# Performance work log

Hardware: AMD Instinct MI355X
Metric: run time of the kernel (lower is better)

## Reference

```python
import jax, jax.numpy as jnp
import numpy as np


def setup_inputs() -> dict:
    key = jax.random.key(0)
    k1, k2 = jax.random.split(key)
    x = jax.random.normal(k1, (16, 1024, 256), dtype=jnp.float32)
    codebooks = jax.random.normal(k2, (8, 1024, 256), dtype=jnp.float32)
    return {"x": x, "codebooks": codebooks}


def _mse(a, b):
    return jnp.mean((a - b) ** 2)


def reference(x, codebooks):
    b, s, d = x.shape
    num_codebooks = codebooks.shape[0]
    xf = x.reshape(-1, d)  # [N, d], N = b*s
    res = xf
    quant = jnp.zeros_like(xf)
    loss_cd = jnp.float32(0.0)
    loss_enc = jnp.float32(0.0)
    encs = []
    for i in range(num_codebooks):  # small fixed loop over sequential RVQ stages
        cb = codebooks[i]  # [cd_size, d]
        # squared euclidean distance; argmin is invariant to the sqrt in cdist(p=2)
        d2 = (jnp.sum(res * res, axis=-1, keepdims=True)
              - 2.0 * (res @ cb.T)
              + jnp.sum(cb * cb, axis=-1))  # [N, cd_size]
        enc = jnp.argmin(d2, axis=-1)  # [N]
        nearest = cb[enc]  # [N, d]
        loss_cd = loss_cd + _mse(jax.lax.stop_gradient(res), nearest)
        loss_enc = loss_enc + _mse(res, jax.lax.stop_gradient(nearest))
        res = res - nearest
        quant = quant + nearest
        encs.append(enc)
    discrete_enc = jnp.stack(encs, axis=-1).astype(jnp.float32).reshape(b, s, num_codebooks)
    # straight-through: quantised = residual + sg(quant - residual)
    quantised = res + jax.lax.stop_gradient(quant - res)
    return loss_cd, loss_enc, discrete_enc, quantised.reshape(b, s, d)
```

## Files before the change

kernel.cpp:

```cpp
#include <hip/hip_runtime.h>


#define D 256
#define NCB 1024
#define NROW 16384
#define STAGES 8
#define NELEM 4194304
#define ENC_OFF 2
#define QUANT_OFF 131074

#define SBR 64
#define SBC 128
#define KD 32
#define APITCH 260
#define BPITCH 36

__device__ __forceinline__ double wave_sum(double t) {
#pragma unroll
    for (int off = 1; off < 64; off <<= 1) t += __shfl_xor(t, off);
    return t;
}

__global__ __launch_bounds__(256)
void cn_kernel(const float* __restrict__ cb_all, double* __restrict__ cn64,
               float* __restrict__ cn32) {
    int c = blockIdx.x * 256 + threadIdx.x;
    const float* row = cb_all + (size_t)c * D;
    double s = 0.0;
    for (int k = 0; k < D; ++k) { double a = (double)row[k]; s = fma(a, a, s); }
    cn64[c] = s;
    cn32[c] = (float)s;
}

__global__ __launch_bounds__(256, 1)
void screen_kernel(const float* __restrict__ resv, const float* __restrict__ cbs,
                   const float* __restrict__ cn32s, int2* __restrict__ ti_buf) {
    __shared__ float a_t[SBR * APITCH];
    __shared__ float b_t[2][SBC * BPITCH];

    const int tid = threadIdx.x;
    const int tc  = tid & 15;
    const int tr  = tid >> 4;
    const int k4  = tid & 7;
    const int cb0 = tid >> 3;
    const long rowbase = (long)blockIdx.x * SBR;

#pragma unroll
    for (int i = 0; i < 16; ++i) {
        int e4 = tid + 256 * i;
        int r = e4 >> 6, kk = e4 & 63;
        *(float4*)&a_t[r * APITCH + kk * 4] =
            *(const float4*)(resv + (rowbase + r) * D + kk * 4);
    }

    float4 P0, P1, P2, P3;
#define BFETCH(T) do { int cc_ = (T) >> 3, dc_ = (T) & 7;                    \
        const float* s_ = cbs + (size_t)(cc_ * SBC) * D + dc_ * KD + k4 * 4; \
        P0 = *(const float4*)(s_ + (size_t)(cb0     ) * D);                  \
        P1 = *(const float4*)(s_ + (size_t)(cb0 + 32) * D);                  \
        P2 = *(const float4*)(s_ + (size_t)(cb0 + 64) * D);                  \
        P3 = *(const float4*)(s_ + (size_t)(cb0 + 96) * D); } while (0)
#define BCOMMIT(BUF) do { float* d_ = &b_t[BUF][cb0 * BPITCH + k4 * 4];      \
        *(float4*)(d_               ) = P0;                                  \
        *(float4*)(d_ + 32 * BPITCH ) = P1;                                  \
        *(float4*)(d_ + 64 * BPITCH ) = P2;                                  \
        *(float4*)(d_ + 96 * BPITCH ) = P3; } while (0)

    BFETCH(0);
    BCOMMIT(0);

    float ts1[4], ts2[4]; int ti1[4], ti2[4];
#pragma unroll
    for (int i = 0; i < 4; ++i) { ts1[i] = 3.4e38f; ts2[i] = 3.4e38f; ti1[i] = 0; ti2[i] = 0; }

    for (int cc = 0; cc < 8; ++cc) {
        float acc[4][8];
#pragma unroll
        for (int i = 0; i < 4; ++i)
#pragma unroll
            for (int j = 0; j < 8; ++j) acc[i][j] = 0.f;

        for (int dc = 0; dc < 8; ++dc) {
            const int t = cc * 8 + dc;
            __syncthreads();
            if (t < 63) BFETCH(t + 1);

            const float* bb   = b_t[t & 1];
            const float* arow = &a_t[(tr * 4) * APITCH + dc * KD];
#pragma unroll
            for (int kq = 0; kq < 8; ++kq) {
                float4 A[4], B[8];
#pragma unroll
                for (int i = 0; i < 4; ++i)
                    A[i] = *(const float4*)&arow[i * APITCH + kq * 4];
#pragma unroll
                for (int j = 0; j < 8; ++j)
                    B[j] = *(const float4*)&bb[(j * 16 + tc) * BPITCH + kq * 4];
#pragma unroll
                for (int i = 0; i < 4; ++i)
#pragma unroll
                    for (int j = 0; j < 8; ++j) {
                        acc[i][j] = fmaf(A[i].x, B[j].x, acc[i][j]);
                        acc[i][j] = fmaf(A[i].y, B[j].y, acc[i][j]);
                        acc[i][j] = fmaf(A[i].z, B[j].z, acc[i][j]);
                        acc[i][j] = fmaf(A[i].w, B[j].w, acc[i][j]);
                    }
            }
            if (t < 63) BCOMMIT((t + 1) & 1);
        }

#pragma unroll
        for (int j = 0; j < 8; ++j) {
            int c = cc * SBC + j * 16 + tc;
            float cnv = cn32s[c];
#pragma unroll
            for (int i = 0; i < 4; ++i) {
                float s = cnv - 2.0f * acc[i][j];
                if (s < ts1[i])      { ts2[i] = ts1[i]; ti2[i] = ti1[i]; ts1[i] = s; ti1[i] = c; }
                else if (s < ts2[i]) { ts2[i] = s; ti2[i] = c; }
            }
        }
    }

#pragma unroll
    for (int off = 1; off < 16; off <<= 1) {
#pragma unroll
        for (int i = 0; i < 4; ++i) {
            float os1 = __shfl_xor(ts1[i], off); int oi1 = __shfl_xor(ti1[i], off);
            float os2 = __shfl_xor(ts2[i], off); int oi2 = __shfl_xor(ti2[i], off);
            float a1 = ts1[i], a2 = ts2[i]; int b1 = ti1[i], b2 = ti2[i];
            if (os1 < a1 || (os1 == a1 && oi1 < b1)) { a2 = a1; b2 = b1; a1 = os1; b1 = oi1; }
            else if (os1 < a2 || (os1 == a2 && oi1 < b2)) { a2 = os1; b2 = oi1; }
            if (os2 < a1 || (os2 == a1 && oi2 < b1)) { a2 = a1; b2 = b1; a1 = os2; b1 = oi2; }
            else if (os2 < a2 || (os2 == a2 && oi2 < b2)) { a2 = os2; b2 = oi2; }
            ts1[i] = a1; ti1[i] = b1; ts2[i] = a2; ti2[i] = b2;
        }
    }
    if (tc == 0) {
#pragma unroll
        for (int i = 0; i < 4; ++i)
            ti_buf[rowbase + tr * 4 + i] = make_int2(ti1[i], ti2[i]);
    }
}

__global__ __launch_bounds__(256)
void rescue_kernel(const float* __restrict__ x, const float* __restrict__ cb_all,
                   const double* __restrict__ cn64s, const int2* __restrict__ ti_buf,
                   float* __restrict__ out, double* __restrict__ loss_acc, int stage) {
    const int lane = threadIdx.x & 63;
    const long row = (long)blockIdx.x * 4 + (threadIdx.x >> 6);
    float* encf  = out + ENC_OFF;
    float* res32 = out + QUANT_OFF;

    double v[4];
    {
        float4 xv = *(const float4*)(x + row * D + lane * 4);
        v[0] = xv.x; v[1] = xv.y; v[2] = xv.z; v[3] = xv.w;
    }
    for (int j = 0; j < stage; ++j) {
        int e = (int)encf[row * STAGES + j];
        float4 c4 = *(const float4*)(cb_all + ((size_t)j * NCB + e) * D + lane * 4);
        v[0] -= (double)c4.x; v[1] -= (double)c4.y; v[2] -= (double)c4.z; v[3] -= (double)c4.w;
    }
    double rn = wave_sum(((v[0]*v[0] + v[1]*v[1]) + (v[2]*v[2] + v[3]*v[3])));

    const int2 cand = ti_buf[row];
    const float4 cb0 = *(const float4*)(cb_all + ((size_t)stage * NCB + cand.x) * D + lane * 4);
    const float4 cb1 = *(const float4*)(cb_all + ((size_t)stage * NCB + cand.y) * D + lane * 4);
    double p0 = fma(v[0], (double)cb0.x, fma(v[1], (double)cb0.y,
                fma(v[2], (double)cb0.z, v[3] * (double)cb0.w)));
    double p1 = fma(v[0], (double)cb1.x, fma(v[1], (double)cb1.y,
                fma(v[2], (double)cb1.z, v[3] * (double)cb1.w)));
    double dot0 = wave_sum(p0);
    double dot1 = wave_sum(p1);
    double dA = (rn - 2.0 * dot0) + cn64s[cand.x];
    double dB = (rn - 2.0 * dot1) + cn64s[cand.y];

    double b1, b2; int j1, j2;
    if (dB < dA || (dB == dA && cand.y < cand.x)) { b1 = dB; j1 = cand.y; b2 = dA; j2 = cand.x; }
    else                                          { b1 = dA; j1 = cand.x; b2 = dB; j2 = cand.y; }
    double delta = ldexp(1.0, ilogb(b1) - 23);
    int chosen = j1; double cd2 = b1;
    if ((b2 - b1) < delta && j2 < j1) { chosen = j2; cd2 = b2; }

    float4 cc4 = (chosen == cand.x) ? cb0 : cb1;
    float4 o;
    o.x = (float)(v[0] - (double)cc4.x);
    o.y = (float)(v[1] - (double)cc4.y);
    o.z = (float)(v[2] - (double)cc4.z);
    o.w = (float)(v[3] - (double)cc4.w);
    *(float4*)(res32 + row * D + lane * 4) = o;

    if (lane == 0) {
        encf[row * STAGES + stage] = (float)chosen;
        atomicAdd(loss_acc, cd2);
    }
}

__global__ __launch_bounds__(256)
void final_kernel(const float* __restrict__ x, const double* __restrict__ acc,
                  float* __restrict__ out) {
    long i0 = (long)blockIdx.x * 256 + threadIdx.x;
    if (i0 == 0) {
        float l = (float)(acc[0] / (double)NELEM);
        out[0] = l;
        out[1] = l;
    }
    float* q = out + QUANT_OFF;
    long stride = (long)gridDim.x * 256;
    for (long e = i0; e < NELEM / 4; e += stride) {
        float4 xv = ((const float4*)x)[e];
        float4 rv = ((const float4*)q)[e];
        float4 o;
        o.x = xv.x - rv.x; o.y = xv.y - rv.y; o.z = xv.z - rv.z; o.w = xv.w - rv.w;
        ((float4*)q)[e] = o;
    }
}

extern "C" void kernel_launch(void* const* d_in, const int* in_sizes, int n_in,
                              void* d_out, int out_size, void* d_ws, size_t ws_size,
                              hipStream_t stream) {
    const float* x  = (const float*)d_in[0];
    const float* cb = (const float*)d_in[1];
    float* out = (float*)d_out;

    double* cn64     = (double*)d_ws;
    float*  cn32     = (float*)(cn64 + 8192);
    int2*   ti_buf   = (int2*)(cn32 + 8192);
    double* loss_acc = (double*)(ti_buf + NROW);

    hipMemsetAsync(loss_acc, 0, sizeof(double), stream);
    cn_kernel<<<32, 256, 0, stream>>>(cb, cn64, cn32);

    for (int s = 0; s < STAGES; ++s) {
        const float* resv = (s == 0) ? x : (out + QUANT_OFF);
        screen_kernel<<<NROW / SBR, 256, 0, stream>>>(
            resv, cb + (size_t)s * NCB * D, cn32 + s * NCB, ti_buf);
        rescue_kernel<<<NROW / 4, 256, 0, stream>>>(
            x, cb, cn64 + s * NCB, ti_buf, out, loss_acc, s);
    }

    final_kernel<<<2048, 256, 0, stream>>>(x, loss_acc, out);
}
```

Before: 3.583 ms.

## Shrink screen tiles for occupancy and replace per-row loss atomics with array reduce

The screen kernel's row tile is halved to 32 rows, with threads remapped to 8x32 and a 4x4 register tile instead of 4x8. This doubles the grid to 512 blocks and allows two blocks per CU, the aim being better occupancy on many CUs at the cost of less register reuse per B load. The rescue kernel now loads its earlier encodings up front into an unrolled array, and writes per-row losses to a buffer instead of issuing a double atomicAdd per row. A separate reduction kernel then sums that buffer, which removes atomic contention but adds a launch and extra workspace.

Result: faster. 3.506 ms (-2.1%).

```diff
diff --git a/kernel.cpp b/kernel.cpp
--- a/kernel.cpp
+++ b/kernel.cpp
@@ -9,7 +9,7 @@
 #define ENC_OFF 2
 #define QUANT_OFF 131074
 
-#define SBR 64
+#define SBR 32
 #define SBC 128
 #define KD 32
 #define APITCH 260
@@ -32,21 +32,21 @@
     cn32[c] = (float)s;
 }
 
-__global__ __launch_bounds__(256, 1)
+__global__ __launch_bounds__(256, 2)
 void screen_kernel(const float* __restrict__ resv, const float* __restrict__ cbs,
                    const float* __restrict__ cn32s, int2* __restrict__ ti_buf) {
     __shared__ float a_t[SBR * APITCH];
     __shared__ float b_t[2][SBC * BPITCH];
 
     const int tid = threadIdx.x;
-    const int tc  = tid & 15;
-    const int tr  = tid >> 4;
+    const int tc  = tid & 31;
+    const int tr  = tid >> 5;
     const int k4  = tid & 7;
     const int cb0 = tid >> 3;
     const long rowbase = (long)blockIdx.x * SBR;
 
 #pragma unroll
-    for (int i = 0; i < 16; ++i) {
+    for (int i = 0; i < 8; ++i) {
         int e4 = tid + 256 * i;
         int r = e4 >> 6, kk = e4 & 63;
         *(float4*)&a_t[r * APITCH + kk * 4] =
@@ -74,11 +74,11 @@
     for (int i = 0; i < 4; ++i) { ts1[i] = 3.4e38f; ts2[i] = 3.4e38f; ti1[i] = 0; ti2[i] = 0; }
 
     for (int cc = 0; cc < 8; ++cc) {
-        float acc[4][8];
+        float acc[4][4];
 #pragma unroll
         for (int i = 0; i < 4; ++i)
 #pragma unroll
-            for (int j = 0; j < 8; ++j) acc[i][j] = 0.f;
+            for (int j = 0; j < 4; ++j) acc[i][j] = 0.f;
 
         for (int dc = 0; dc < 8; ++dc) {
             const int t = cc * 8 + dc;
@@ -89,17 +89,17 @@
             const float* arow = &a_t[(tr * 4) * APITCH + dc * KD];
 #pragma unroll
             for (int kq = 0; kq < 8; ++kq) {
-                float4 A[4], B[8];
+                float4 A[4], B[4];
 #pragma unroll
                 for (int i = 0; i < 4; ++i)
                     A[i] = *(const float4*)&arow[i * APITCH + kq * 4];
 #pragma unroll
-                for (int j = 0; j < 8; ++j)
-                    B[j] = *(const float4*)&bb[(j * 16 + tc) * BPITCH + kq * 4];
+                for (int j = 0; j < 4; ++j)
+                    B[j] = *(const float4*)&bb[(j * 32 + tc) * BPITCH + kq * 4];
 #pragma unroll
                 for (int i = 0; i < 4; ++i)
 #pragma unroll
-                    for (int j = 0; j < 8; ++j) {
+                    for (int j = 0; j < 4; ++j) {
                         acc[i][j] = fmaf(A[i].x, B[j].x, acc[i][j]);
                         acc[i][j] = fmaf(A[i].y, B[j].y, acc[i][j]);
                         acc[i][j] = fmaf(A[i].z, B[j].z, acc[i][j]);
@@ -110,8 +110,8 @@
         }
 
 #pragma unroll
-        for (int j = 0; j < 8; ++j) {
-            int c = cc * SBC + j * 16 + tc;
+        for (int j = 0; j < 4; ++j) {
+            int c = cc * SBC + j * 32 + tc;
             float cnv = cn32s[c];
 #pragma unroll
             for (int i = 0; i < 4; ++i) {
@@ -123,7 +123,7 @@
     }
 
 #pragma unroll
-    for (int off = 1; off < 16; off <<= 1) {
+    for (int off = 1; off < 32; off <<= 1) {
 #pragma unroll
         for (int i = 0; i < 4; ++i) {
             float os1 = __shfl_xor(ts1[i], off); int oi1 = __shfl_xor(ti1[i], off);
@@ -146,21 +146,31 @@
 __global__ __launch_bounds__(256)
 void rescue_kernel(const float* __restrict__ x, const float* __restrict__ cb_all,
                    const double* __restrict__ cn64s, const int2* __restrict__ ti_buf,
-                   float* __restrict__ out, double* __restrict__ loss_acc, int stage) {
+                   float* __restrict__ out, double* __restrict__ loss_arr, int stage) {
     const int lane = threadIdx.x & 63;
     const long row = (long)blockIdx.x * 4 + (threadIdx.x >> 6);
     float* encf  = out + ENC_OFF;
     float* res32 = out + QUANT_OFF;
 
+    int e[STAGES];
+#pragma unroll
+    for (int j = 0; j < STAGES; ++j) {
+        float ef = encf[row * STAGES + j];
+        e[j] = (j < stage) ? (int)ef : 0;
+    }
+
     double v[4];
     {
         float4 xv = *(const float4*)(x + row * D + lane * 4);
         v[0] = xv.x; v[1] = xv.y; v[2] = xv.z; v[3] = xv.w;
     }
-    for (int j = 0; j < stage; ++j) {
-        int e = (int)encf[row * STAGES + j];
-        float4 c4 = *(const float4*)(cb_all + ((size_t)j * NCB + e) * D + lane * 4);
-        v[0] -= (double)c4.x; v[1] -= (double)c4.y; v[2] -= (double)c4.z; v[3] -= (double)c4.w;
+#pragma unroll
+    for (int j = 0; j < STAGES; ++j) {
+        if (j < stage) {
+            float4 c4 = *(const float4*)(cb_all + ((size_t)j * NCB + e[j]) * D + lane * 4);
+            v[0] -= (double)c4.x; v[1] -= (double)c4.y;
+            v[2] -= (double)c4.z; v[3] -= (double)c4.w;
+        }
     }
     double rn = wave_sum(((v[0]*v[0] + v[1]*v[1]) + (v[2]*v[2] + v[3]*v[3])));
 
@@ -193,8 +203,19 @@
 
     if (lane == 0) {
         encf[row * STAGES + stage] = (float)chosen;
-        atomicAdd(loss_acc, cd2);
-    }
+        loss_arr[(size_t)stage * NROW + row] = cd2;
+    }
+}
+
+__global__ __launch_bounds__(256)
+void loss_reduce(const double* __restrict__ loss_arr, double* __restrict__ acc) {
+    long i = (long)blockIdx.x * 256 + threadIdx.x;
+    double s = 0.0;
+    long total = (long)NROW * STAGES;
+    long stride = (long)gridDim.x * 256;
+    for (long e = i; e < total; e += stride) s += loss_arr[e];
+    s = wave_sum(s);
+    if ((threadIdx.x & 63) == 0) atomicAdd(acc, s);
 }
 
 __global__ __launch_bounds__(256)
@@ -227,7 +248,8 @@
     double* cn64     = (double*)d_ws;
     float*  cn32     = (float*)(cn64 + 8192);
     int2*   ti_buf   = (int2*)(cn32 + 8192);
-    double* loss_acc = (double*)(ti_buf + NROW);
+    double* loss_arr = (double*)(ti_buf + NROW);
+    double* loss_acc = loss_arr + (size_t)NROW * STAGES;
 
     hipMemsetAsync(loss_acc, 0, sizeof(double), stream);
     cn_kernel<<<32, 256, 0, stream>>>(cb, cn64, cn32);
@@ -237,8 +259,9 @@
         screen_kernel<<<NROW / SBR, 256, 0, stream>>>(
             resv, cb + (size_t)s * NCB * D, cn32 + s * NCB, ti_buf);
         rescue_kernel<<<NROW / 4, 256, 0, stream>>>(
-            x, cb, cn64 + s * NCB, ti_buf, out, loss_acc, s);
-    }
-
+            x, cb, cn64 + s * NCB, ti_buf, out, loss_arr, s);
+    }
+
+    loss_reduce<<<64, 256, 0, stream>>>(loss_arr, loss_acc);
     final_kernel<<<2048, 256, 0, stream>>>(x, loss_acc, out);
 }
```
